# Performance work log

Hardware: AMD Instinct MI355X
Metric: run time of the kernel (lower is better)

## Reference

```python
import jax, jax.numpy as jnp
import numpy as np

N, E, F, H, C = 50000, 800000, 128, 64, 40
EPS = 1e-12


def _l2norm(x):
    n = jnp.sqrt(jnp.sum(x * x, axis=-1, keepdims=True))
    return x / jnp.maximum(n, EPS)


def _sage_conv(x, edge_index, Wl, bl, Wr, num_nodes):
    # PyG SAGEConv, aggr='mean', normalize=True:
    #   out = lin_l(mean_{j in N(i)} x_j) + lin_r(x_i); out = l2_normalize(out)
    src, dst = edge_index[0], edge_index[1]
    msg = x[src]  # [E, F] gathered neighbor features
    agg = jax.ops.segment_sum(msg, dst, num_segments=num_nodes)
    cnt = jax.ops.segment_sum(jnp.ones((edge_index.shape[1],), x.dtype), dst,
                              num_segments=num_nodes)
    mean = agg / jnp.maximum(cnt, 1.0)[:, None]  # zero-in-degree nodes -> 0
    out = mean @ Wl + bl + x @ Wr
    return _l2norm(out)


def setup_inputs() -> dict:
    key = jax.random.key(0)
    ks = jax.random.split(key, 10)
    s = lambda fan_in: 1.0 / np.sqrt(fan_in)
    x = jax.random.normal(ks[0], (N, F), dtype=jnp.float32)
    edge_index = jax.random.randint(ks[1], (2, E), 0, N, dtype=jnp.int64)
    # conv1: SAGEConv(F -> H); lin_l has bias, lin_r has no bias
    Wl1 = jax.random.uniform(ks[2], (F, H), jnp.float32, -s(F), s(F))
    bl1 = jnp.zeros((H,), jnp.float32)
    Wr1 = jax.random.uniform(ks[3], (F, H), jnp.float32, -s(F), s(F))
    # lin1: Linear(F + H -> H)
    Wlin = jax.random.uniform(ks[4], (F + H, H), jnp.float32, -s(F + H), s(F + H))
    blin = jax.random.uniform(ks[5], (H,), jnp.float32, -s(F + H), s(F + H))
    # conv2: SAGEConv(H -> C)
    Wl2 = jax.random.uniform(ks[6], (H, C), jnp.float32, -s(H), s(H))
    bl2 = jnp.zeros((C,), jnp.float32)
    Wr2 = jax.random.uniform(ks[7], (H, C), jnp.float32, -s(H), s(H))
    return {"x": x, "edge_index": edge_index,
            "Wl1": Wl1, "bl1": bl1, "Wr1": Wr1,
            "Wlin": Wlin, "blin": blin,
            "Wl2": Wl2, "bl2": bl2, "Wr2": Wr2}


def reference(x, edge_index, Wl1, bl1, Wr1, Wlin, blin, Wl2, bl2, Wr2):
    hidden = jax.nn.relu(_sage_conv(x, edge_index, Wl1, bl1, Wr1, N))
    h = jax.nn.relu(jnp.concatenate([x, hidden], axis=1) @ Wlin + blin)
    # dropout is identity in eval mode
    out = _sage_conv(h, edge_index, Wl2, bl2, Wr2, N)
    return out
```

## Files before the change

### kernel.cpp

```cpp
#include <hip/hip_runtime.h>

static constexpr int NN = 50000;
static constexpr int NE = 800000;
static constexpr int F  = 128;
static constexpr int H  = 64;
static constexpr int C  = 40;

static constexpr int NB_BK = 8;
static constexpr int NCH   = 32;
static constexpr int ECH   = NE / NCH;
static constexpr int NBK   = NN / NB_BK;
static constexpr int NCSR  = NB_BK * NCH;
static constexpr int NT64  = (NN + 63) / 64;

typedef __attribute__((ext_vector_type(8))) short bf16x8;
typedef __attribute__((ext_vector_type(8))) unsigned short u16x8;
typedef __attribute__((ext_vector_type(4))) float f32x4;

__device__ inline unsigned short f2bf(float f) {
  unsigned int u = __builtin_bit_cast(unsigned int, f);
  u = (u + 0x7fff + ((u >> 16) & 1)) >> 16;
  return (unsigned short)u;
}
__device__ inline float bf2f(unsigned short u) {
  return __builtin_bit_cast(float, (unsigned int)u << 16);
}


__device__ void hist_body(int bid, const int* __restrict__ ei,
                          int* __restrict__ hist, int* __restrict__ counter) {
  __shared__ int cnt[NBK];
  int i = bid & 7;
  int j = bid >> 3;
  for (int t = threadIdx.x; t < NBK; t += 256) cnt[t] = 0;
  __syncthreads();
  if (bid == 0 && threadIdx.x == 0) *counter = 0;
  int lo = i * NBK;
  const int* dst = ei + NE + j * ECH;
  for (int base = threadIdx.x * 4; base < ECH; base += 256 * 4) {
    int4 d4 = *reinterpret_cast<const int4*>(dst + base);
    if ((unsigned)(d4.x - lo) < (unsigned)NBK) atomicAdd(&cnt[d4.x - lo], 1);
    if ((unsigned)(d4.y - lo) < (unsigned)NBK) atomicAdd(&cnt[d4.y - lo], 1);
    if ((unsigned)(d4.z - lo) < (unsigned)NBK) atomicAdd(&cnt[d4.z - lo], 1);
    if ((unsigned)(d4.w - lo) < (unsigned)NBK) atomicAdd(&cnt[d4.w - lo], 1);
  }
  __syncthreads();
  int* hrow = hist + (size_t)j * NN + lo;
  for (int t = threadIdx.x; t < NBK; t += 256) hrow[t] = cnt[t];
}

__device__ void cvt_body(int bid, const float* __restrict__ x,
                         unsigned short* __restrict__ xb) {
  int id = bid * 256 + threadIdx.x;
  int ns = NT64 * 256;
  for (int i = id; i < NN * F / 4; i += ns) {
    float4 v = reinterpret_cast<const float4*>(x)[i];
    ushort4 o = {f2bf(v.x), f2bf(v.y), f2bf(v.z), f2bf(v.w)};
    reinterpret_cast<ushort4*>(xb)[i] = o;
  }
}

__device__ void scan_body(int bid, int* __restrict__ hist,
                          int* __restrict__ deg, int* __restrict__ start,
                          int* __restrict__ counter) {
  int lane = threadIdx.x & 63;
  int wid  = (bid * 256 + threadIdx.x) >> 6;
  int nchunks = (NN + 63) >> 6;
  if (wid >= nchunks) return;
  int n = (wid << 6) + lane;
  int d = 0;
  if (n < NN) {
    int run = 0;
#pragma unroll
    for (int j = 0; j < NCH; ++j) {
      int v = hist[(size_t)j * NN + n];
      hist[(size_t)j * NN + n] = run;
      run += v;
    }
    d = run;
  }
  int inc = d;
#pragma unroll
  for (int off = 1; off < 64; off <<= 1) {
    int t = __shfl_up(inc, off, 64);
    if (lane >= off) inc += t;
  }
  int total = __shfl(inc, 63, 64);
  int base = 0;
  if (lane == 63) base = atomicAdd(counter, total);
  base = __shfl(base, 63, 64);
  if (n < NN) {
    deg[n]   = d;
    start[n] = base + inc - d;
  }
}

__device__ inline void packW(const float* __restrict__ W, int J, int NT,
                             unsigned short* __restrict__ Wf, int idx) {
  int j  = idx & 7;
  int l  = (idx >> 3) & 63;
  int nt = (idx >> 9) % NT;
  int s  = idx / (512 * NT);
  int k  = s * 32 + (l >> 4) * 8 + j;
  int n  = nt * 16 + (l & 15);
  float v = (n < J) ? W[k * J + n] : 0.f;
  Wf[idx] = f2bf(v);
}

__device__ void prep_body(int bid,
                          const float* __restrict__ Wl1, const float* __restrict__ Wr1,
                          const float* __restrict__ Wlin,
                          const float* __restrict__ Wl2, const float* __restrict__ Wr2,
                          unsigned short* __restrict__ Wf1l, unsigned short* __restrict__ Wf1r,
                          unsigned short* __restrict__ Wflin,
                          unsigned short* __restrict__ Wf2l, unsigned short* __restrict__ Wf2r) {
  int id0 = bid * 256 + threadIdx.x;
  int ns  = 48 * 256;
  for (int i = id0; i < 4 * 4 * 512; i += ns) packW(Wl1, 64, 4, Wf1l, i);
  for (int i = id0; i < 4 * 4 * 512; i += ns) packW(Wr1, 64, 4, Wf1r, i);
  for (int i = id0; i < 6 * 4 * 512; i += ns) packW(Wlin, 64, 4, Wflin, i);
  for (int i = id0; i < 2 * 4 * 512; i += ns) packW(Wl2, 40, 4, Wf2l, i);
  for (int i = id0; i < 2 * 4 * 512; i += ns) packW(Wr2, 40, 4, Wf2r, i);
}

__device__ void fill2_body(int bid, const int* __restrict__ ei,
                           const int* __restrict__ hist,
                           const int* __restrict__ start,
                           int* __restrict__ csr_src) {
  __shared__ int fill[NBK];
  int i = bid & 7;
  int j = bid >> 3;
  int lo = i * NBK;
  const int* hrow = hist + (size_t)j * NN + lo;
  for (int t = threadIdx.x; t < NBK; t += 256) fill[t] = start[lo + t] + hrow[t];
  __syncthreads();
  const int* srcp = ei + j * ECH;
  const int* dstp = ei + NE + j * ECH;
  for (int base = threadIdx.x * 4; base < ECH; base += 256 * 4) {
    int4 s4 = *reinterpret_cast<const int4*>(srcp + base);
    int4 d4 = *reinterpret_cast<const int4*>(dstp + base);
    if ((unsigned)(d4.x - lo) < (unsigned)NBK) { int p = atomicAdd(&fill[d4.x - lo], 1); csr_src[p] = s4.x; }
    if ((unsigned)(d4.y - lo) < (unsigned)NBK) { int p = atomicAdd(&fill[d4.y - lo], 1); csr_src[p] = s4.y; }
    if ((unsigned)(d4.z - lo) < (unsigned)NBK) { int p = atomicAdd(&fill[d4.z - lo], 1); csr_src[p] = s4.z; }
    if ((unsigned)(d4.w - lo) < (unsigned)NBK) { int p = atomicAdd(&fill[d4.w - lo], 1); csr_src[p] = s4.w; }
  }
}


template <int K1, int K2, int JOUT, int NT, int NMAT, bool BIAS, bool RELU, bool OUTBF>
__device__ void mf_body(int bid,
                        const unsigned short* __restrict__ A1,
                        const unsigned short* __restrict__ A2,
                        const unsigned short* __restrict__ Wf0,
                        const unsigned short* __restrict__ Wf1,
                        const float* __restrict__ bias,
                        void* __restrict__ Y0v, void* __restrict__ Y1v) {
  constexpr int K   = K1 + K2;
  constexpr int NKS = K / 32;
  int lane = threadIdx.x & 63;
  int w    = __builtin_amdgcn_readfirstlane(threadIdx.x >> 6);
  int m    = lane & 15;
  int kg   = lane >> 4;
  int n0   = bid * 64;
  int row  = n0 + w * 16 + m;
  int rowc = row < NN ? row : NN - 1;

  f32x4 acc[NMAT][NT];
#pragma unroll
  for (int mt = 0; mt < NMAT; ++mt)
#pragma unroll
    for (int nt = 0; nt < NT; ++nt) acc[mt][nt] = {0.f, 0.f, 0.f, 0.f};

#pragma unroll
  for (int s = 0; s < NKS; ++s) {
    const unsigned short* Ab; int rs, koff;
    if (s * 32 < K1) { Ab = A1; rs = K1; koff = s * 32; }
    else             { Ab = A2; rs = K2; koff = s * 32 - K1; }
    bf16x8 a = *reinterpret_cast<const bf16x8*>(Ab + (size_t)rowc * rs + koff + kg * 8);
#pragma unroll
    for (int mt = 0; mt < NMAT; ++mt) {
      const unsigned short* Wf = (NMAT == 2 && mt) ? Wf1 : Wf0;
#pragma unroll
      for (int nt = 0; nt < NT; ++nt) {
        bf16x8 b = *reinterpret_cast<const bf16x8*>(Wf + (size_t)((s * NT + nt) * 64 + lane) * 8);
        acc[mt][nt] = __builtin_amdgcn_mfma_f32_16x16x32_bf16(a, b, acc[mt][nt], 0, 0, 0);
      }
    }
  }

#pragma unroll
  for (int mt = 0; mt < NMAT; ++mt) {
    void* Yv = (NMAT == 2 && mt) ? Y1v : Y0v;
#pragma unroll
    for (int nt = 0; nt < NT; ++nt) {
      int gc = nt * 16 + m;
      bool cv = gc < JOUT;
      float bb = (BIAS && cv) ? bias[gc] : 0.f;
#pragma unroll
      for (int r = 0; r < 4; ++r) {
        int grow = n0 + w * 16 + kg * 4 + r;
        if (grow < NN && cv) {
          float v = acc[mt][nt][r] + bb;
          if (RELU) v = fmaxf(v, 0.f);
          if (OUTBF) ((unsigned short*)Yv)[(size_t)grow * JOUT + gc] = f2bf(v);
          else       ((float*)Yv)[(size_t)grow * JOUT + gc] = v;
        }
      }
    }
  }
}


__global__ __launch_bounds__(256) void k_p1(const int* __restrict__ ei,
                                            int* __restrict__ hist,
                                            int* __restrict__ counter,
                                            const float* __restrict__ x,
                                            unsigned short* __restrict__ xb) {
  if (blockIdx.x < NCSR) hist_body(blockIdx.x, ei, hist, counter);
  else                   cvt_body(blockIdx.x - NCSR, x, xb);
}

__global__ __launch_bounds__(256) void k_p2(int* __restrict__ hist,
                                            int* __restrict__ deg,
                                            int* __restrict__ start,
                                            int* __restrict__ counter,
                                            const float* Wl1, const float* Wr1,
                                            const float* Wlin,
                                            const float* Wl2, const float* Wr2,
                                            unsigned short* Wf1l, unsigned short* Wf1r,
                                            unsigned short* Wflin,
                                            unsigned short* Wf2l, unsigned short* Wf2r) {
  if (blockIdx.x < 196) scan_body(blockIdx.x, hist, deg, start, counter);
  else prep_body(blockIdx.x - 196, Wl1, Wr1, Wlin, Wl2, Wr2,
                 Wf1l, Wf1r, Wflin, Wf2l, Wf2r);
}

__global__ __launch_bounds__(256) void k_p3(const int* __restrict__ ei,
                                            const int* __restrict__ hist,
                                            const int* __restrict__ start,
                                            int* __restrict__ csr_src,
                                            const unsigned short* __restrict__ xb,
                                            const unsigned short* __restrict__ Wf1l,
                                            const unsigned short* __restrict__ Wf1r,
                                            unsigned short* __restrict__ p1b,
                                            unsigned short* __restrict__ q1b) {
  if (blockIdx.x < NCSR) fill2_body(blockIdx.x, ei, hist, start, csr_src);
  else mf_body<F, 0, H, 4, 2, false, false, true>(blockIdx.x - NCSR, xb, nullptr,
                                                  Wf1l, Wf1r, nullptr, p1b, q1b);
}

template <int K1, int K2, int JOUT, int NT, int NMAT, bool BIAS, bool RELU, bool OUTBF>
__global__ __launch_bounds__(256) void k_mf(const unsigned short* __restrict__ A1,
                                            const unsigned short* __restrict__ A2,
                                            const unsigned short* __restrict__ Wf0,
                                            const unsigned short* __restrict__ Wf1,
                                            const float* __restrict__ bias,
                                            void* __restrict__ Y0v,
                                            void* __restrict__ Y1v) {
  mf_body<K1, K2, JOUT, NT, NMAT, BIAS, RELU, OUTBF>(blockIdx.x, A1, A2, Wf0, Wf1,
                                                     bias, Y0v, Y1v);
}


template <int JCR, bool RELU, bool OUTBF>
__global__ __launch_bounds__(256) void k_aggv(const unsigned short* __restrict__ p,
                                              const unsigned short* __restrict__ q,
                                              const float* __restrict__ bl,
                                              const int* __restrict__ deg,
                                              const int* __restrict__ start,
                                              const int* __restrict__ csr_src,
                                              void* __restrict__ outp) {
  constexpr int ST = 64;
  int lane = threadIdx.x & 63;
  int e = lane >> 3, c = lane & 7;
  int wid = (blockIdx.x * blockDim.x + threadIdx.x) >> 6;
  int nw  = (gridDim.x * blockDim.x) >> 6;

  float blv[8];
#pragma unroll
  for (int j = 0; j < 8; ++j) {
    int f = c * 8 + j;
    blv[j] = (f < JCR) ? bl[f] : 0.f;
  }

  for (int node = wid; node < NN; node += nw) {
    int d  = __builtin_amdgcn_readfirstlane(deg[node]);
    int st = __builtin_amdgcn_readfirstlane(start[node]);
    float a0[8], a1[8];
#pragma unroll
    for (int j = 0; j < 8; ++j) { a0[j] = 0.f; a1[j] = 0.f; }
    int r = 0;
    for (; r + 16 <= d; r += 16) {
      int i0 = csr_src[st + r + e];
      int i1 = csr_src[st + r + 8 + e];
      u16x8 v0 = *reinterpret_cast<const u16x8*>(p + (size_t)i0 * ST + c * 8);
      u16x8 v1 = *reinterpret_cast<const u16x8*>(p + (size_t)i1 * ST + c * 8);
#pragma unroll
      for (int j = 0; j < 8; ++j) { a0[j] += bf2f(v0[j]); a1[j] += bf2f(v1[j]); }
    }
    if (r + 8 <= d) {
      int i0 = csr_src[st + r + e];
      u16x8 v0 = *reinterpret_cast<const u16x8*>(p + (size_t)i0 * ST + c * 8);
#pragma unroll
      for (int j = 0; j < 8; ++j) a0[j] += bf2f(v0[j]);
      r += 8;
    }
    int rem = d - r;
    if (rem > 0) {
      int ec = e < rem ? e : rem - 1;
      int i0 = csr_src[st + r + ec];
      u16x8 v0 = *reinterpret_cast<const u16x8*>(p + (size_t)i0 * ST + c * 8);
      if (e < rem) {
#pragma unroll
        for (int j = 0; j < 8; ++j) a0[j] += bf2f(v0[j]);
      }
    }
#pragma unroll
    for (int j = 0; j < 8; ++j) a0[j] += a1[j];
#pragma unroll
    for (int ms = 8; ms <= 32; ms <<= 1)
#pragma unroll
      for (int j = 0; j < 8; ++j) a0[j] += __shfl_xor(a0[j], ms, 64);

    float inv = 1.f / fmaxf((float)d, 1.f);
    u16x8 qv = *reinterpret_cast<const u16x8*>(q + (size_t)node * ST + c * 8);
    float v[8];
    float ss = 0.f;
#pragma unroll
    for (int j = 0; j < 8; ++j) {
      int f = c * 8 + j;
      float t = a0[j] * inv + blv[j] + bf2f(qv[j]);
      if (f >= JCR) t = 0.f;
      v[j] = t;
      ss += t * t;
    }
#pragma unroll
    for (int ms = 1; ms <= 4; ms <<= 1) ss += __shfl_xor(ss, ms, 64);
    float rn = 1.f / fmaxf(sqrtf(ss), 1e-12f);

    if (e == 0 && c * 8 < JCR) {
      if (OUTBF) {
        u16x8 o;
#pragma unroll
        for (int j = 0; j < 8; ++j) {
          float t = v[j] * rn;
          if (RELU) t = fmaxf(t, 0.f);
          o[j] = f2bf(t);
        }
        *reinterpret_cast<u16x8*>((unsigned short*)outp + (size_t)node * JCR + c * 8) = o;
      } else {
        float* op = (float*)outp + (size_t)node * JCR + c * 8;
#pragma unroll
        for (int j = 0; j < 8; j += 4) {
          float4 o = {v[j] * rn, v[j + 1] * rn, v[j + 2] * rn, v[j + 3] * rn};
          if (RELU) {
            o.x = fmaxf(o.x, 0.f); o.y = fmaxf(o.y, 0.f);
            o.z = fmaxf(o.z, 0.f); o.w = fmaxf(o.w, 0.f);
          }
          *reinterpret_cast<float4*>(op + j) = o;
        }
      }
    }
  }
}


static inline size_t align256(size_t x) { return (x + 255) & ~(size_t)255; }

extern "C" void kernel_launch(void* const* d_in, const int* in_sizes, int n_in,
                              void* d_out, int out_size, void* d_ws, size_t ws_size,
                              hipStream_t stream) {
  const float* x    = (const float*)d_in[0];
  const int*   ei   = (const int*)d_in[1];
  const float* Wl1  = (const float*)d_in[2];
  const float* bl1  = (const float*)d_in[3];
  const float* Wr1  = (const float*)d_in[4];
  const float* Wlin = (const float*)d_in[5];
  const float* blin = (const float*)d_in[6];
  const float* Wl2  = (const float*)d_in[7];
  const float* bl2  = (const float*)d_in[8];
  const float* Wr2  = (const float*)d_in[9];
  float* out = (float*)d_out;

  char* w = (char*)d_ws;
  size_t off = 0;
  int* deg     = (int*)(w + off); off += align256((size_t)NN * 4);
  int* start   = (int*)(w + off); off += align256((size_t)NN * 4);
  int* counter = (int*)(w + off); off += 256;
  int* csr_src = (int*)(w + off); off += align256((size_t)NE * 4);
  int* hist    = (int*)(w + off); off += align256((size_t)NCH * NN * 4);
  unsigned short* xb      = (unsigned short*)(w + off); off += align256((size_t)NN * F * 2);
  unsigned short* hiddenb = (unsigned short*)(w + off); off += align256((size_t)NN * H * 2);
  unsigned short* hb      = (unsigned short*)(w + off); off += align256((size_t)NN * H * 2);
  unsigned short* p1b = (unsigned short*)(w + off); off += align256((size_t)NN * 64 * 2);
  unsigned short* q1b = (unsigned short*)(w + off); off += align256((size_t)NN * 64 * 2);
  unsigned short* p2b = (unsigned short*)(w + off); off += align256((size_t)NN * 64 * 2);
  unsigned short* q2b = (unsigned short*)(w + off); off += align256((size_t)NN * 64 * 2);
  unsigned short* Wf1l  = (unsigned short*)(w + off); off += align256(4 * 4 * 512 * 2);
  unsigned short* Wf1r  = (unsigned short*)(w + off); off += align256(4 * 4 * 512 * 2);
  unsigned short* Wflin = (unsigned short*)(w + off); off += align256(6 * 4 * 512 * 2);
  unsigned short* Wf2l  = (unsigned short*)(w + off); off += align256(2 * 4 * 512 * 2);
  unsigned short* Wf2r  = (unsigned short*)(w + off); off += align256(2 * 4 * 512 * 2);

  const int T = 256;

  k_p1<<<NCSR + NT64, T, 0, stream>>>(ei, hist, counter, x, xb);
  k_p2<<<244, T, 0, stream>>>(hist, deg, start, counter,
                              Wl1, Wr1, Wlin, Wl2, Wr2,
                              Wf1l, Wf1r, Wflin, Wf2l, Wf2r);
  k_p3<<<NCSR + NT64, T, 0, stream>>>(ei, hist, start, csr_src,
                                      xb, Wf1l, Wf1r, p1b, q1b);
  k_aggv<H, true, true><<<2048, T, 0, stream>>>(p1b, q1b, bl1, deg, start, csr_src, hiddenb);
  k_mf<F, H, H, 4, 1, true, true, true><<<NT64, T, 0, stream>>>(
      xb, hiddenb, Wflin, nullptr, blin, hb, nullptr);
  k_mf<H, 0, 64, 4, 2, false, false, true><<<NT64, T, 0, stream>>>(
      hb, nullptr, Wf2l, Wf2r, nullptr, p2b, q2b);
  k_aggv<C, false, false><<<2048, T, 0, stream>>>(p2b, q2b, bl2, deg, start, csr_src, out);
}
```

Measured before the change: 205.1 us.

## Fuse lin1 and conv2 projections into one kernel; prefetch CSR indices in aggregation

New measurement: 215.3 us. 5.0% more time.

```diff
diff --git a/kernel.cpp b/kernel.cpp
--- a/kernel.cpp
+++ b/kernel.cpp
@@ -249,16 +249,83 @@
                                                   Wf1l, Wf1r, nullptr, p1b, q1b);
 }
 
-template <int K1, int K2, int JOUT, int NT, int NMAT, bool BIAS, bool RELU, bool OUTBF>
-__global__ __launch_bounds__(256) void k_mf(const unsigned short* __restrict__ A1,
-                                            const unsigned short* __restrict__ A2,
-                                            const unsigned short* __restrict__ Wf0,
-                                            const unsigned short* __restrict__ Wf1,
-                                            const float* __restrict__ bias,
-                                            void* __restrict__ Y0v,
-                                            void* __restrict__ Y1v) {
-  mf_body<K1, K2, JOUT, NT, NMAT, BIAS, RELU, OUTBF>(blockIdx.x, A1, A2, Wf0, Wf1,
-                                                     bias, Y0v, Y1v);
+
+__global__ __launch_bounds__(256) void k_lin2(const unsigned short* __restrict__ xb,
+                                              const unsigned short* __restrict__ hiddenb,
+                                              const unsigned short* __restrict__ Wflin,
+                                              const unsigned short* __restrict__ Wf2l,
+                                              const unsigned short* __restrict__ Wf2r,
+                                              const float* __restrict__ blin,
+                                              unsigned short* __restrict__ p2b,
+                                              unsigned short* __restrict__ q2b) {
+  constexpr int PAD = 72;
+  __shared__ unsigned short hs[64 * PAD];
+  int lane = threadIdx.x & 63;
+  int w    = __builtin_amdgcn_readfirstlane(threadIdx.x >> 6);
+  int m    = lane & 15;
+  int kg   = lane >> 4;
+  int n0   = blockIdx.x * 64;
+  int row  = n0 + w * 16 + m;
+  int rowc = row < NN ? row : NN - 1;
+
+  f32x4 acc[4];
+#pragma unroll
+  for (int nt = 0; nt < 4; ++nt) acc[nt] = {0.f, 0.f, 0.f, 0.f};
+#pragma unroll
+  for (int s = 0; s < 6; ++s) {
+    const unsigned short* Ab; int rs, koff;
+    if (s < 4) { Ab = xb;      rs = F; koff = s * 32; }
+    else       { Ab = hiddenb; rs = H; koff = (s - 4) * 32; }
+    bf16x8 a = *reinterpret_cast<const bf16x8*>(Ab + (size_t)rowc * rs + koff + kg * 8);
+#pragma unroll
+    for (int nt = 0; nt < 4; ++nt) {
+      bf16x8 b = *reinterpret_cast<const bf16x8*>(Wflin + (size_t)((s * 4 + nt) * 64 + lane) * 8);
+      acc[nt] = __builtin_amdgcn_mfma_f32_16x16x32_bf16(a, b, acc[nt], 0, 0, 0);
+    }
+  }
+#pragma unroll
+  for (int nt = 0; nt < 4; ++nt) {
+    int gc = nt * 16 + m;
+    float bb = blin[gc];
+#pragma unroll
+    for (int r = 0; r < 4; ++r) {
+      float v = fmaxf(acc[nt][r] + bb, 0.f);
+      hs[(w * 16 + kg * 4 + r) * PAD + gc] = f2bf(v);
+    }
+  }
+  __syncthreads();
+
+  f32x4 acc2[2][4];
+#pragma unroll
+  for (int mt = 0; mt < 2; ++mt)
+#pragma unroll
+    for (int nt = 0; nt < 4; ++nt) acc2[mt][nt] = {0.f, 0.f, 0.f, 0.f};
+#pragma unroll
+  for (int s = 0; s < 2; ++s) {
+    bf16x8 a = *reinterpret_cast<const bf16x8*>(&hs[(w * 16 + m) * PAD + s * 32 + kg * 8]);
+#pragma unroll
+    for (int mt = 0; mt < 2; ++mt) {
+      const unsigned short* Wf = mt ? Wf2r : Wf2l;
+#pragma unroll
+      for (int nt = 0; nt < 4; ++nt) {
+        bf16x8 b = *reinterpret_cast<const bf16x8*>(Wf + (size_t)((s * 4 + nt) * 64 + lane) * 8);
+        acc2[mt][nt] = __builtin_amdgcn_mfma_f32_16x16x32_bf16(a, b, acc2[mt][nt], 0, 0, 0);
+      }
+    }
+  }
+#pragma unroll
+  for (int mt = 0; mt < 2; ++mt) {
+    unsigned short* Yv = mt ? q2b : p2b;
+#pragma unroll
+    for (int nt = 0; nt < 4; ++nt) {
+      int gc = nt * 16 + m;
+#pragma unroll
+      for (int r = 0; r < 4; ++r) {
+        int grow = n0 + w * 16 + kg * 4 + r;
+        if (grow < NN) Yv[(size_t)grow * 64 + gc] = f2bf(acc2[mt][nt][r]);
+      }
+    }
+  }
 }
 
 
@@ -290,13 +357,22 @@
 #pragma unroll
     for (int j = 0; j < 8; ++j) { a0[j] = 0.f; a1[j] = 0.f; }
     int r = 0;
-    for (; r + 16 <= d; r += 16) {
-      int i0 = csr_src[st + r + e];
-      int i1 = csr_src[st + r + 8 + e];
+    int iA = 0, iB = 0;
+    bool have = (16 <= d);
+    if (have) { iA = csr_src[st + e]; iB = csr_src[st + 8 + e]; }
+    while (have) {
+      int i0 = iA, i1 = iB;
+      int rn = r + 16;
+      bool haveN = (rn + 16 <= d);
+      if (haveN) {
+        iA = csr_src[st + rn + e];
+        iB = csr_src[st + rn + 8 + e];
+      }
       u16x8 v0 = *reinterpret_cast<const u16x8*>(p + (size_t)i0 * ST + c * 8);
       u16x8 v1 = *reinterpret_cast<const u16x8*>(p + (size_t)i1 * ST + c * 8);
 #pragma unroll
       for (int j = 0; j < 8; ++j) { a0[j] += bf2f(v0[j]); a1[j] += bf2f(v1[j]); }
+      r = rn; have = haveN;
     }
     if (r + 8 <= d) {
       int i0 = csr_src[st + r + e];
@@ -336,14 +412,14 @@
     }
 #pragma unroll
     for (int ms = 1; ms <= 4; ms <<= 1) ss += __shfl_xor(ss, ms, 64);
-    float rn = 1.f / fmaxf(sqrtf(ss), 1e-12f);
+    float rn2 = 1.f / fmaxf(sqrtf(ss), 1e-12f);
 
     if (e == 0 && c * 8 < JCR) {
       if (OUTBF) {
         u16x8 o;
 #pragma unroll
         for (int j = 0; j < 8; ++j) {
-          float t = v[j] * rn;
+          float t = v[j] * rn2;
           if (RELU) t = fmaxf(t, 0.f);
           o[j] = f2bf(t);
         }
@@ -352,7 +428,7 @@
         float* op = (float*)outp + (size_t)node * JCR + c * 8;
 #pragma unroll
         for (int j = 0; j < 8; j += 4) {
-          float4 o = {v[j] * rn, v[j + 1] * rn, v[j + 2] * rn, v[j + 3] * rn};
+          float4 o = {v[j] * rn2, v[j + 1] * rn2, v[j + 2] * rn2, v[j + 3] * rn2};
           if (RELU) {
             o.x = fmaxf(o.x, 0.f); o.y = fmaxf(o.y, 0.f);
             o.z = fmaxf(o.z, 0.f); o.w = fmaxf(o.w, 0.f);
@@ -391,7 +467,6 @@
   int* hist    = (int*)(w + off); off += align256((size_t)NCH * NN * 4);
   unsigned short* xb      = (unsigned short*)(w + off); off += align256((size_t)NN * F * 2);
   unsigned short* hiddenb = (unsigned short*)(w + off); off += align256((size_t)NN * H * 2);
-  unsigned short* hb      = (unsigned short*)(w + off); off += align256((size_t)NN * H * 2);
   unsigned short* p1b = (unsigned short*)(w + off); off += align256((size_t)NN * 64 * 2);
   unsigned short* q1b = (unsigned short*)(w + off); off += align256((size_t)NN * 64 * 2);
   unsigned short* p2b = (unsigned short*)(w + off); off += align256((size_t)NN * 64 * 2);
@@ -411,9 +486,6 @@
   k_p3<<<NCSR + NT64, T, 0, stream>>>(ei, hist, start, csr_src,
                                       xb, Wf1l, Wf1r, p1b, q1b);
   k_aggv<H, true, true><<<2048, T, 0, stream>>>(p1b, q1b, bl1, deg, start, csr_src, hiddenb);
-  k_mf<F, H, H, 4, 1, true, true, true><<<NT64, T, 0, stream>>>(
-      xb, hiddenb, Wflin, nullptr, blin, hb, nullptr);
-  k_mf<H, 0, 64, 4, 2, false, false, true><<<NT64, T, 0, stream>>>(
-      hb, nullptr, Wf2l, Wf2r, nullptr, p2b, q2b);
+  k_lin2<<<NT64, T, 0, stream>>>(xb, hiddenb, Wflin, Wf2l, Wf2r, blin, p2b, q2b);
   k_aggv<C, false, false><<<2048, T, 0, stream>>>(p2b, q2b, bl2, deg, start, csr_src, out);
 }
```
